# Kernel tuning notes

Measured on AMD Instinct MI355X. Metric: run time of the kernel, lower is better.

## Reference

```python
import jax, jax.numpy as jnp
import numpy as np

N = 131072          # number of input points
C = 2000            # num_centers (20*5*20 grid)
D = 3               # input_dim
L = 0.2             # length scale: beta = 1/L


def setup_inputs() -> dict:
    key = jax.random.key(0)
    kx, kc, kw = jax.random.split(key, 3)
    # inputs uniform in [-1, 1]^3 to match the center grid domain
    x = jax.random.uniform(kx, (N, D), dtype=jnp.float32, minval=-1.0, maxval=1.0)
    # centers: 20x5x20 meshgrid over [-1,1]^3, flattened to (C, D)
    g1 = jnp.linspace(-1.0, 1.0, 20)
    g2 = jnp.linspace(-1.0, 1.0, 5)
    g3 = jnp.linspace(-1.0, 1.0, 20)
    mesh = jnp.meshgrid(g1, g2, g3, indexing='ij')
    centers = jnp.stack(mesh, axis=-1).reshape(-1, D).astype(jnp.float32)  # (C, D)
    beta = jnp.ones((C,), dtype=jnp.float32) / L                            # (C,)
    # nn.Linear(num_centers, 1, bias=False) with normal(0, 0.1) init
    lin_w = 0.1 * jax.random.normal(kw, (1, C), dtype=jnp.float32)          # (1, C)
    return {"x": x, "centers": centers, "beta": beta, "lin_w": lin_w}


def reference(x, centers, beta, lin_w):
    x2 = jnp.sum(x * x, axis=1, keepdims=True)            # (N, 1)
    c2 = jnp.sum(centers * centers, axis=1)               # (C,)
    distances = x2 + c2 - 2.0 * (x @ centers.T)           # (N, C)
    rbf = jnp.exp(-beta * distances)                      # (N, C)
    sum_rbf = jnp.sum(rbf, axis=1, keepdims=True)         # (N, 1)
    out = (rbf @ lin_w.T) / sum_rbf                       # (N, 1)
    return out
```

## Files before the change

### kernel.cpp

```cpp
#include <hip/hip_runtime.h>


typedef float v2f __attribute__((ext_vector_type(2)));

__global__ __launch_bounds__(256, 4) void rbf_fused(
        const float* __restrict__ x,
        const float* __restrict__ centers,
        const float* __restrict__ beta,
        const float* __restrict__ lin_w,
        float* __restrict__ out,
        int n) {
    __shared__ float wlds[100 * 24];
    __shared__ float cst[90];
    __shared__ float red[4][4][64];

    const int tid  = threadIdx.x;
    const int lane = tid & 63;
    const int wv   = __builtin_amdgcn_readfirstlane(tid >> 6);

    if (tid < 45) {
        const float LOG2E = 1.4426950408889634f;
        float b = beta[0] * LOG2E;
        float gv;
        int k1o, k0o, idx;
        if (tid < 20)      { idx = tid;      gv = centers[3*(idx*100) + 0]; k1o = 0;  k0o = 20; }
        else if (tid < 25) { idx = tid - 20; gv = centers[3*(idx*20)  + 1]; k1o = 40; k0o = 45; }
        else               { idx = tid - 25; gv = centers[3*idx       + 2]; k1o = 50; k0o = 70; }
        cst[k1o + idx] = 2.0f * b * gv;
        cst[k0o + idx] = -b * gv * gv;
    }
    #pragma unroll
    for (int idx = tid; idx < 2000; idx += 256) {
        int i = idx / 100;
        int m = idx - i * 100;
        wlds[m * 24 + i] = lin_w[idx];
    }

    const int pA = blockIdx.x * 128 + lane;
    const int pB = pA + 64;
    const bool vA = (pA < n), vB = (pB < n);

    float a0 = 0.f, a1 = 0.f, a2 = 0.f, b0 = 0.f, b1 = 0.f, b2 = 0.f;
    if (vA) { a0 = x[3*pA]; a1 = x[3*pA+1]; a2 = x[3*pA+2]; }
    if (vB) { b0 = x[3*pB]; b1 = x[3*pB+1]; b2 = x[3*pB+2]; }

    __syncthreads();

    const int kbase = wv * 5;

    v2f EA[10], EB[10];
    #pragma unroll
    for (int i2 = 0; i2 < 10; ++i2) {
        float k1a = cst[2*i2],   k0a = cst[20 + 2*i2];
        float k1b = cst[2*i2+1], k0b = cst[20 + 2*i2+1];
        EA[i2].x = __builtin_amdgcn_exp2f(fmaf(k1a, a0, k0a));
        EA[i2].y = __builtin_amdgcn_exp2f(fmaf(k1b, a0, k0b));
        EB[i2].x = __builtin_amdgcn_exp2f(fmaf(k1a, b0, k0a));
        EB[i2].y = __builtin_amdgcn_exp2f(fmaf(k1b, b0, k0b));
    }
    float fA[5], fB[5], gA[5], gB[5];
    #pragma unroll
    for (int j = 0; j < 5; ++j) {
        float k1 = cst[40 + j], k0 = cst[45 + j];
        fA[j] = __builtin_amdgcn_exp2f(fmaf(k1, a1, k0));
        fB[j] = __builtin_amdgcn_exp2f(fmaf(k1, b1, k0));
    }
    #pragma unroll
    for (int kk = 0; kk < 5; ++kk) {
        float k1 = cst[50 + kbase + kk], k0 = cst[70 + kbase + kk];
        gA[kk] = __builtin_amdgcn_exp2f(fmaf(k1, a2, k0));
        gB[kk] = __builtin_amdgcn_exp2f(fmaf(k1, b2, k0));
    }

    float numA = 0.f, numB = 0.f;
    #pragma unroll
    for (int j = 0; j < 5; ++j) {
        #pragma unroll
        for (int kk = 0; kk < 5; ++kk) {
            const float4* wr = (const float4*)&wlds[(j*20 + kbase + kk) * 24];
            float4 w0 = wr[0], w1 = wr[1], w2 = wr[2], w3 = wr[3], w4 = wr[4];
            v2f W[10] = { {w0.x,w0.y}, {w0.z,w0.w}, {w1.x,w1.y}, {w1.z,w1.w},
                          {w2.x,w2.y}, {w2.z,w2.w}, {w3.x,w3.y}, {w3.z,w3.w},
                          {w4.x,w4.y}, {w4.z,w4.w} };
            v2f tA2 = W[0] * EA[0];
            v2f tB2 = W[0] * EB[0];
            #pragma unroll
            for (int i2 = 1; i2 < 10; ++i2) {
                tA2 = __builtin_elementwise_fma(W[i2], EA[i2], tA2);
                tB2 = __builtin_elementwise_fma(W[i2], EB[i2], tB2);
            }
            numA = fmaf(tA2.x + tA2.y, fA[j] * gA[kk], numA);
            numB = fmaf(tB2.x + tB2.y, fB[j] * gB[kk], numB);
        }
    }

    float sgA = 0.f, sgB = 0.f;
    #pragma unroll
    for (int kk = 0; kk < 5; ++kk) { sgA += gA[kk]; sgB += gB[kk]; }

    if (wv > 0) {
        red[wv][0][lane] = numA;  red[wv][1][lane] = sgA;
        red[wv][2][lane] = numB;  red[wv][3][lane] = sgB;
    }
    __syncthreads();
    if (wv == 0) {
        #pragma unroll
        for (int w2i = 1; w2i < 4; ++w2i) {
            numA += red[w2i][0][lane];  sgA += red[w2i][1][lane];
            numB += red[w2i][2][lane];  sgB += red[w2i][3][lane];
        }
        v2f seA2 = EA[0], seB2 = EB[0];
        #pragma unroll
        for (int i2 = 1; i2 < 10; ++i2) { seA2 += EA[i2]; seB2 += EB[i2]; }
        float seA = seA2.x + seA2.y, seB = seB2.x + seB2.y;
        float sfA = 0.f, sfB = 0.f;
        #pragma unroll
        for (int j = 0; j < 5; ++j) { sfA += fA[j]; sfB += fB[j]; }
        if (vA) out[pA] = numA / (seA * sfA * sgA);
        if (vB) out[pB] = numB / (seB * sfB * sgB);
    }
}

extern "C" void kernel_launch(void* const* d_in, const int* in_sizes, int n_in,
                              void* d_out, int out_size, void* d_ws, size_t ws_size,
                              hipStream_t stream) {
    const float* x       = (const float*)d_in[0];
    const float* centers = (const float*)d_in[1];
    const float* beta    = (const float*)d_in[2];
    const float* lin_w   = (const float*)d_in[3];
    float* out = (float*)d_out;

    int n = in_sizes[0] / 3;

    int main_blocks = (n + 127) / 128;
    rbf_fused<<<main_blocks, 256, 0, stream>>>(x, centers, beta, lin_w, out, n);
}
```

Measured before the change: 68.86 us.

## Read RBF weights via scalar loads and split waves over the first grid axis

```diff
diff --git a/kernel.cpp b/kernel.cpp
--- a/kernel.cpp
+++ b/kernel.cpp
@@ -1,7 +1,20 @@
 #include <hip/hip_runtime.h>
 
 
-typedef float v2f __attribute__((ext_vector_type(2)));
+typedef float v2f  __attribute__((ext_vector_type(2)));
+typedef float v4f  __attribute__((ext_vector_type(4)));
+typedef float v16f __attribute__((ext_vector_type(16)));
+
+__device__ __forceinline__ v2f mk2(float lo, float hi) { v2f r; r.x = lo; r.y = hi; return r; }
+
+template<int OFF>
+__device__ __forceinline__ void sload20(const float* __restrict__ base, v16f& a, v4f& b) {
+    asm("s_load_dwordx16 %0, %2, %c3\n\t"
+        "s_load_dwordx4  %1, %2, %c4\n\t"
+        "s_waitcnt lgkmcnt(0)"
+        : "=s"(a), "=s"(b)
+        : "s"(base), "i"(OFF), "i"(OFF + 64));
+}
 
 __global__ __launch_bounds__(256, 4) void rbf_fused(
         const float* __restrict__ x,
@@ -10,13 +23,12 @@
         const float* __restrict__ lin_w,
         float* __restrict__ out,
         int n) {
-    __shared__ float wlds[100 * 24];
     __shared__ float cst[90];
     __shared__ float red[4][4][64];
 
     const int tid  = threadIdx.x;
     const int lane = tid & 63;
-    const int wv   = __builtin_amdgcn_readfirstlane(tid >> 6);
+    const int wvu  = __builtin_amdgcn_readfirstlane(tid >> 6);
 
     if (tid < 45) {
         const float LOG2E = 1.4426950408889634f;
@@ -29,12 +41,6 @@
         cst[k1o + idx] = 2.0f * b * gv;
         cst[k0o + idx] = -b * gv * gv;
     }
-    #pragma unroll
-    for (int idx = tid; idx < 2000; idx += 256) {
-        int i = idx / 100;
-        int m = idx - i * 100;
-        wlds[m * 24 + i] = lin_w[idx];
-    }
 
     const int pA = blockIdx.x * 128 + lane;
     const int pB = pA + 64;
@@ -46,76 +52,82 @@
 
     __syncthreads();
 
-    const int kbase = wv * 5;
+    const float* wbase = lin_w + wvu * 500;
 
-    v2f EA[10], EB[10];
-    #pragma unroll
-    for (int i2 = 0; i2 < 10; ++i2) {
-        float k1a = cst[2*i2],   k0a = cst[20 + 2*i2];
-        float k1b = cst[2*i2+1], k0b = cst[20 + 2*i2+1];
-        EA[i2].x = __builtin_amdgcn_exp2f(fmaf(k1a, a0, k0a));
-        EA[i2].y = __builtin_amdgcn_exp2f(fmaf(k1b, a0, k0b));
-        EB[i2].x = __builtin_amdgcn_exp2f(fmaf(k1a, b0, k0a));
-        EB[i2].y = __builtin_amdgcn_exp2f(fmaf(k1b, b0, k0b));
-    }
-    float fA[5], fB[5], gA[5], gB[5];
+    float fA[5], fB[5];
     #pragma unroll
     for (int j = 0; j < 5; ++j) {
         float k1 = cst[40 + j], k0 = cst[45 + j];
         fA[j] = __builtin_amdgcn_exp2f(fmaf(k1, a1, k0));
         fB[j] = __builtin_amdgcn_exp2f(fmaf(k1, b1, k0));
     }
+    v2f GA[10], GB[10];
     #pragma unroll
-    for (int kk = 0; kk < 5; ++kk) {
-        float k1 = cst[50 + kbase + kk], k0 = cst[70 + kbase + kk];
-        gA[kk] = __builtin_amdgcn_exp2f(fmaf(k1, a2, k0));
-        gB[kk] = __builtin_amdgcn_exp2f(fmaf(k1, b2, k0));
+    for (int p = 0; p < 10; ++p) {
+        float k1x = cst[50 + 2*p],     k0x = cst[70 + 2*p];
+        float k1y = cst[50 + 2*p + 1], k0y = cst[70 + 2*p + 1];
+        GA[p].x = __builtin_amdgcn_exp2f(fmaf(k1x, a2, k0x));
+        GA[p].y = __builtin_amdgcn_exp2f(fmaf(k1y, a2, k0y));
+        GB[p].x = __builtin_amdgcn_exp2f(fmaf(k1x, b2, k0x));
+        GB[p].y = __builtin_amdgcn_exp2f(fmaf(k1y, b2, k0y));
     }
 
-    float numA = 0.f, numB = 0.f;
-    #pragma unroll
-    for (int j = 0; j < 5; ++j) {
-        #pragma unroll
-        for (int kk = 0; kk < 5; ++kk) {
-            const float4* wr = (const float4*)&wlds[(j*20 + kbase + kk) * 24];
-            float4 w0 = wr[0], w1 = wr[1], w2 = wr[2], w3 = wr[3], w4 = wr[4];
-            v2f W[10] = { {w0.x,w0.y}, {w0.z,w0.w}, {w1.x,w1.y}, {w1.z,w1.w},
-                          {w2.x,w2.y}, {w2.z,w2.w}, {w3.x,w3.y}, {w3.z,w3.w},
-                          {w4.x,w4.y}, {w4.z,w4.w} };
-            v2f tA2 = W[0] * EA[0];
-            v2f tB2 = W[0] * EB[0];
-            #pragma unroll
-            for (int i2 = 1; i2 < 10; ++i2) {
-                tA2 = __builtin_elementwise_fma(W[i2], EA[i2], tA2);
-                tB2 = __builtin_elementwise_fma(W[i2], EB[i2], tB2);
-            }
-            numA = fmaf(tA2.x + tA2.y, fA[j] * gA[kk], numA);
-            numB = fmaf(tB2.x + tB2.y, fB[j] * gB[kk], numB);
-        }
-    }
+    float numA = 0.f, numB = 0.f, seA = 0.f, seB = 0.f;
+    float uA = 0.f, uB = 0.f;
 
-    float sgA = 0.f, sgB = 0.f;
-    #pragma unroll
-    for (int kk = 0; kk < 5; ++kk) { sgA += gA[kk]; sgB += gB[kk]; }
+#define RBF_ROW(R) do { \
+        v16f W16; v4f W4; \
+        sload20<((R)/5)*400 + ((R)%5)*80>(wbase, W16, W4); \
+        v2f w, tA, tB; \
+        w = mk2(W16[0],  W16[1]);  tA = w * GA[0]; tB = w * GB[0]; \
+        w = mk2(W16[2],  W16[3]);  tA = __builtin_elementwise_fma(w, GA[1], tA); tB = __builtin_elementwise_fma(w, GB[1], tB); \
+        w = mk2(W16[4],  W16[5]);  tA = __builtin_elementwise_fma(w, GA[2], tA); tB = __builtin_elementwise_fma(w, GB[2], tB); \
+        w = mk2(W16[6],  W16[7]);  tA = __builtin_elementwise_fma(w, GA[3], tA); tB = __builtin_elementwise_fma(w, GB[3], tB); \
+        w = mk2(W16[8],  W16[9]);  tA = __builtin_elementwise_fma(w, GA[4], tA); tB = __builtin_elementwise_fma(w, GB[4], tB); \
+        w = mk2(W16[10], W16[11]); tA = __builtin_elementwise_fma(w, GA[5], tA); tB = __builtin_elementwise_fma(w, GB[5], tB); \
+        w = mk2(W16[12], W16[13]); tA = __builtin_elementwise_fma(w, GA[6], tA); tB = __builtin_elementwise_fma(w, GB[6], tB); \
+        w = mk2(W16[14], W16[15]); tA = __builtin_elementwise_fma(w, GA[7], tA); tB = __builtin_elementwise_fma(w, GB[7], tB); \
+        w = mk2(W4[0],   W4[1]);   tA = __builtin_elementwise_fma(w, GA[8], tA); tB = __builtin_elementwise_fma(w, GB[8], tB); \
+        w = mk2(W4[2],   W4[3]);   tA = __builtin_elementwise_fma(w, GA[9], tA); tB = __builtin_elementwise_fma(w, GB[9], tB); \
+        uA = fmaf(fA[(R)%5], tA.x + tA.y, uA); \
+        uB = fmaf(fB[(R)%5], tB.x + tB.y, uB); \
+    } while (0)
 
-    if (wv > 0) {
-        red[wv][0][lane] = numA;  red[wv][1][lane] = sgA;
-        red[wv][2][lane] = numB;  red[wv][3][lane] = sgB;
+#define RBF_FOLD(II) do { \
+        float k1 = cst[5*wvu + (II)], k0 = cst[20 + 5*wvu + (II)]; \
+        float eAv = __builtin_amdgcn_exp2f(fmaf(k1, a0, k0)); \
+        float eBv = __builtin_amdgcn_exp2f(fmaf(k1, b0, k0)); \
+        numA = fmaf(eAv, uA, numA); numB = fmaf(eBv, uB, numB); \
+        seA += eAv; seB += eBv; uA = 0.f; uB = 0.f; \
+    } while (0)
+
+    RBF_ROW(0);  RBF_ROW(1);  RBF_ROW(2);  RBF_ROW(3);  RBF_ROW(4);   RBF_FOLD(0);
+    RBF_ROW(5);  RBF_ROW(6);  RBF_ROW(7);  RBF_ROW(8);  RBF_ROW(9);   RBF_FOLD(1);
+    RBF_ROW(10); RBF_ROW(11); RBF_ROW(12); RBF_ROW(13); RBF_ROW(14);  RBF_FOLD(2);
+    RBF_ROW(15); RBF_ROW(16); RBF_ROW(17); RBF_ROW(18); RBF_ROW(19);  RBF_FOLD(3);
+    RBF_ROW(20); RBF_ROW(21); RBF_ROW(22); RBF_ROW(23); RBF_ROW(24);  RBF_FOLD(4);
+
+#undef RBF_ROW
+#undef RBF_FOLD
+
+    if (wvu > 0) {
+        red[wvu][0][lane] = numA;  red[wvu][1][lane] = seA;
+        red[wvu][2][lane] = numB;  red[wvu][3][lane] = seB;
     }
     __syncthreads();
-    if (wv == 0) {
+    if (wvu == 0) {
         #pragma unroll
-        for (int w2i = 1; w2i < 4; ++w2i) {
-            numA += red[w2i][0][lane];  sgA += red[w2i][1][lane];
-            numB += red[w2i][2][lane];  sgB += red[w2i][3][lane];
+        for (int w2 = 1; w2 < 4; ++w2) {
+            numA += red[w2][0][lane];  seA += red[w2][1][lane];
+            numB += red[w2][2][lane];  seB += red[w2][3][lane];
         }
-        v2f seA2 = EA[0], seB2 = EB[0];
-        #pragma unroll
-        for (int i2 = 1; i2 < 10; ++i2) { seA2 += EA[i2]; seB2 += EB[i2]; }
-        float seA = seA2.x + seA2.y, seB = seB2.x + seB2.y;
         float sfA = 0.f, sfB = 0.f;
         #pragma unroll
         for (int j = 0; j < 5; ++j) { sfA += fA[j]; sfB += fB[j]; }
+        v2f sg2A = GA[0], sg2B = GB[0];
+        #pragma unroll
+        for (int p = 1; p < 10; ++p) { sg2A += GA[p]; sg2B += GB[p]; }
+        float sgA = sg2A.x + sg2A.y, sgB = sg2B.x + sg2B.y;
         if (vA) out[pA] = numA / (seA * sfA * sgA);
         if (vB) out[pB] = numB / (seB * sfB * sgB);
     }
```

Result: faster. 67.41 us (-2.1%).
